# Kernel optimization log

Hardware: AMD Instinct MI355X
Metric: run time of the kernel (lower is better)

## Reference

```python
import jax, jax.numpy as jnp
import numpy as np

C, N, D, DQ, K = 8, 16384, 1024, 128, 128  # clusters, patches/cluster, feat dim, q dim, top_k per cluster


def setup_inputs() -> dict:
    key = jax.random.key(0)
    ks = jax.random.split(key, 4)
    s = 0.02
    return {
        "cluster_features": jax.random.normal(ks[0], (C, N, D), jnp.float32),
        "key_feats": jax.random.normal(ks[1], (C, 1, D), jnp.float32),
        "Wq": jax.random.normal(ks[2], (D, DQ), jnp.float32) * s,
        "bq": jnp.zeros((DQ,), jnp.float32),
        "Wv": jax.random.normal(ks[3], (D, D), jnp.float32) * s,
        "bv": jnp.zeros((D,), jnp.float32),
    }


def _ranking_topk(feats, key_feat, Wq, bq, Wv, bv):
    # feats: [n, d], key_feat: [1, d]
    Q = feats @ Wq + bq                     # [n, DQ]
    qk = key_feat @ Wq + bq                 # [1, DQ]
    A = Q @ qk.T                            # [n, 1] attention scores
    A = jax.nn.softmax(A / jnp.sqrt(jnp.float32(DQ)), axis=0)
    top_vals, top_idx = jax.lax.top_k(A[:, 0], K)   # sorted descending, like torch.topk
    top_feats = feats[top_idx]              # [K, d] gather
    V = top_feats @ Wv + bv                 # value projection on gathered subset only
    A_ = jax.nn.softmax(top_vals[:, None] / jnp.sqrt(jnp.float32(D)), axis=0)  # [K, 1]
    fusion = (A_.T @ V)[0]                  # [d] fused weighted sum
    return top_feats, fusion


def reference(cluster_features, key_feats, Wq, bq, Wv, bv):
    top_feats, fusion = jax.vmap(
        lambda f, kf: _ranking_topk(f, kf, Wq, bq, Wv, bv)
    )(cluster_features, key_feats)
    # concat per-cluster selections; C*K == num_sample_feature so no padding branch
    selected_features = top_feats.reshape(C * K, D)
    cluster_fusion_feature = fusion         # [C, D]
    return selected_features, cluster_fusion_feature
```

## Files before the change

### kernel.cpp

```cpp
#include <hip/hip_runtime.h>

#define C_CLUST 8
#define N_PAT   16384
#define D_FEAT  1024
#define DQ_DIM  128
#define K_TOP   128
#define NCHUNK  32
#define CHROWS  512

#define INV_S128 0.08838834764831844055
#define INV_S1024 0.03125

__device__ inline unsigned f2key(float f) {
    unsigned u = __float_as_uint(f);
    return (u & 0x80000000u) ? ~u : (u | 0x80000000u);
}
__device__ inline float key2f(unsigned k) {
    unsigned u = (k & 0x80000000u) ? (k ^ 0x80000000u) : ~k;
    return __uint_as_float(u);
}

__global__ __launch_bounds__(1024) void prep_kernel(
    const float* __restrict__ key_feats,
    const float* __restrict__ Wq,
    const float* __restrict__ bq,
    double* __restrict__ r,
    double* __restrict__ b0)
{
    __shared__ float keyrow[D_FEAT];
    __shared__ double part[1024];
    __shared__ double qk_lds[DQ_DIM];
    const int b = blockIdx.x;
    const int c = b >> 3, g = b & 7;
    const int tid = threadIdx.x;
    const int lane = tid & 63, wv = tid >> 6;

    keyrow[tid] = key_feats[c * D_FEAT + tid];
    __syncthreads();

    {
        const int j = tid & 127, s = tid >> 7;
        double acc = 0.0;
        for (int d = s; d < D_FEAT; d += 8)
            acc += (double)keyrow[d] * (double)Wq[d * DQ_DIM + j];
        part[s * DQ_DIM + j] = acc;
    }
    __syncthreads();
    if (tid < DQ_DIM) {
        double v = part[tid];
#pragma unroll
        for (int s2 = 1; s2 < 8; ++s2) v += part[s2 * DQ_DIM + tid];
        qk_lds[tid] = v + (double)bq[tid];
    }
    __syncthreads();

    if (g == 0 && wv == 0) {
        double p = (double)bq[lane] * qk_lds[lane] + (double)bq[64 + lane] * qk_lds[64 + lane];
#pragma unroll
        for (int o = 32; o > 0; o >>= 1) p += __shfl_xor(p, o, 64);
        if (lane == 0) b0[c] = p;
    }

    {
        const double q0 = qk_lds[lane], q1 = qk_lds[64 + lane];
        const int d0 = g * 128 + wv * 8;
#pragma unroll
        for (int i = 0; i < 8; ++i) {
            const int d = d0 + i;
            double a = (double)Wq[d * DQ_DIM + lane] * q0
                     + (double)Wq[d * DQ_DIM + 64 + lane] * q1;
#pragma unroll
            for (int o = 32; o > 0; o >>= 1) a += __shfl_xor(a, o, 64);
            if (lane == 0) r[c * D_FEAT + d] = a;
        }
    }
}

__global__ __launch_bounds__(256) void score_kernel(
    const float* __restrict__ feats,
    const double* __restrict__ r,
    const double* __restrict__ b0,
    float* __restrict__ scores)
{
    const int w    = blockIdx.x * 4 + (threadIdx.x >> 6);
    const int lane = threadIdx.x & 63;
    const int c  = w >> 10;
    const int n0 = (w & 1023) * 16;

    const double* rp = r + c * D_FEAT;
    double rr[16];
#pragma unroll
    for (int it = 0; it < 4; ++it)
#pragma unroll
        for (int j = 0; j < 4; ++j)
            rr[it * 4 + j] = rp[it * 256 + lane * 4 + j];
    const double bb = b0[c];

    const float4* fbase = (const float4*)(feats + (size_t)(c * N_PAT + n0) * D_FEAT);
    float* sout = scores + c * N_PAT + n0;

    for (int rI = 0; rI < 16; rI += 2) {
        const float4* fp0 = fbase + (size_t)(rI + 0) * 256;
        const float4* fp1 = fbase + (size_t)(rI + 1) * 256;
        double acc0 = 0.0, acc1 = 0.0;
#pragma unroll
        for (int it = 0; it < 4; ++it) {
            float4 f0 = fp0[it * 64 + lane];
            float4 f1 = fp1[it * 64 + lane];
            acc0 += (double)f0.x * rr[it * 4 + 0];
            acc0 += (double)f0.y * rr[it * 4 + 1];
            acc0 += (double)f0.z * rr[it * 4 + 2];
            acc0 += (double)f0.w * rr[it * 4 + 3];
            acc1 += (double)f1.x * rr[it * 4 + 0];
            acc1 += (double)f1.y * rr[it * 4 + 1];
            acc1 += (double)f1.z * rr[it * 4 + 2];
            acc1 += (double)f1.w * rr[it * 4 + 3];
        }
#pragma unroll
        for (int o = 32; o > 0; o >>= 1) {
            acc0 += __shfl_xor(acc0, o, 64);
            acc1 += __shfl_xor(acc1, o, 64);
        }
        if (lane == 0) {
            sout[rI + 0] = (float)(acc0 + bb);
            sout[rI + 1] = (float)(acc1 + bb);
        }
    }
}

__global__ __launch_bounds__(256) void chunksort_kernel(
    const float* __restrict__ scores,
    unsigned long long* __restrict__ cand,
    unsigned* __restrict__ mxkey,
    double* __restrict__ Ssum)
{
    const int b = blockIdx.x;
    const int c = b >> 5, chunk = b & 31;
    const int tid = threadIdx.x;
    const int lane = tid & 63, wv = tid >> 6;

    __shared__ unsigned long long su[CHROWS];
    __shared__ unsigned ured[4];
    __shared__ double dred[4];
    __shared__ unsigned bmax_s;

    const int base = c * N_PAT + chunk * CHROWS;
    const float s0 = scores[base + tid];
    const float s1 = scores[base + 256 + tid];
    const unsigned k0 = f2key(s0), k1 = f2key(s1);
    su[tid]       = ((unsigned long long)k0 << 32) | (unsigned)(~(unsigned)(chunk * CHROWS + tid));
    su[tid + 256] = ((unsigned long long)k1 << 32) | (unsigned)(~(unsigned)(chunk * CHROWS + 256 + tid));

    unsigned mk = max(k0, k1);
#pragma unroll
    for (int o = 32; o > 0; o >>= 1) mk = max(mk, __shfl_xor(mk, o, 64));
    if (lane == 0) ured[wv] = mk;
    __syncthreads();
    if (tid == 0) bmax_s = max(max(ured[0], ured[1]), max(ured[2], ured[3]));
    __syncthreads();
    const unsigned kmax = bmax_s;
    const double mx_t = (double)key2f(kmax) * INV_S128;
    double es = (double)__expf((float)((double)s0 * INV_S128 - mx_t))
              + (double)__expf((float)((double)s1 * INV_S128 - mx_t));
#pragma unroll
    for (int o = 32; o > 0; o >>= 1) es += __shfl_xor(es, o, 64);
    if (lane == 0) dred[wv] = es;
    __syncthreads();
    if (tid == 0) {
        Ssum[c * NCHUNK + chunk] = dred[0] + dred[1] + dred[2] + dred[3];
        mxkey[c * NCHUNK + chunk] = kmax;
    }

    for (int k = 2; k <= CHROWS; k <<= 1) {
        for (int j = k >> 1; j > 0; j >>= 1) {
            __syncthreads();
#pragma unroll
            for (int ii = 0; ii < 2; ++ii) {
                const int i = ii * 256 + tid, l = i ^ j;
                if (l > i) {
                    unsigned long long a = su[i], b2 = su[l];
                    const bool desc = ((i & k) == 0);
                    if (desc ? (a < b2) : (a > b2)) { su[i] = b2; su[l] = a; }
                }
            }
        }
    }
    __syncthreads();
    if (tid < K_TOP) cand[(size_t)(c * NCHUNK + chunk) * K_TOP + tid] = su[tid];
}

__global__ __launch_bounds__(256) void gather_merge_kernel(
    const float* __restrict__ feats,
    const unsigned long long* __restrict__ cand,
    const unsigned* __restrict__ mxkey,
    const double* __restrict__ Ssum,
    float* __restrict__ out,
    double* __restrict__ w_part)
{
    const int b = blockIdx.x;
    const int c = b >> 4, quarter = (b >> 2) & 3, ich = b & 3;
    const int tid = threadIdx.x;
    const int lane = tid & 63, wv = tid >> 6;

    __shared__ unsigned long long su2[4096];
    __shared__ double pd[K_TOP];
    __shared__ double sa[K_TOP];
    __shared__ int sidx[K_TOP];
    __shared__ double dred2[2];
    __shared__ double sZ;

#pragma unroll
    for (int k = 0; k < 16; ++k)
        su2[k * 256 + tid] = cand[(size_t)c * 4096 + k * 256 + tid];
    __syncthreads();

    for (int nl = 32; nl > 1; nl >>= 1) {
        const int half = nl >> 1;
        const int total = half * K_TOP;
        unsigned long long tmp[8];
        int cnt = 0;
        for (int i = tid; i < total; i += 256) {
            const int g = i >> 7, li = i & 127;
            unsigned long long a  = su2[(2 * g) * K_TOP + li];
            unsigned long long b2 = su2[(2 * g + 1) * K_TOP + (K_TOP - 1 - li)];
            tmp[cnt++] = a > b2 ? a : b2;
        }
        __syncthreads();
        cnt = 0;
        for (int i = tid; i < total; i += 256) su2[i] = tmp[cnt++];
        __syncthreads();
        for (int j = 64; j > 0; j >>= 1) {
            for (int i = tid; i < total; i += 256) {
                const int li = i & 127, l = li ^ j;
                if (l > li) {
                    const int base = i - li;
                    unsigned long long a = su2[base + li], b2 = su2[base + l];
                    if (a < b2) { su2[base + li] = b2; su2[base + l] = a; }
                }
            }
            __syncthreads();
        }
    }

    const double m_t = (double)key2f((unsigned)(su2[0] >> 32)) * INV_S128;
    if (wv == 0) {
        double z = (lane < NCHUNK)
            ? Ssum[c * NCHUNK + lane] * exp((double)key2f(mxkey[c * NCHUNK + lane]) * INV_S128 - m_t)
            : 0.0;
#pragma unroll
        for (int o = 32; o > 0; o >>= 1) z += __shfl_xor(z, o, 64);
        if (lane == 0) sZ = z;
    }
    __syncthreads();
    const double Z = sZ;
    if (tid < K_TOP) {
        unsigned long long pr = su2[tid];
        sidx[tid] = (int)(~(unsigned)(pr & 0xFFFFFFFFull));
        pd[tid] = exp((double)key2f((unsigned)(pr >> 32)) * INV_S128 - m_t) / Z;
    }
    __syncthreads();
    if (tid < K_TOP) {
        double e = exp((pd[tid] - pd[0]) * INV_S1024);
        double se = e;
#pragma unroll
        for (int o = 32; o > 0; o >>= 1) se += __shfl_xor(se, o, 64);
        if (lane == 0) dred2[wv] = se;
    }
    __syncthreads();
    if (tid < K_TOP) {
        double tot = dred2[0] + dred2[1];
        sa[tid] = exp((pd[tid] - pd[0]) * INV_S1024) / tot;
    }
    __syncthreads();

    const int d = quarter * 256 + tid;
    const float* fc = feats + (size_t)c * N_PAT * D_FEAT + d;
    float* oc = out + ((size_t)c * K_TOP + ich * 32) * D_FEAT + d;
    double a0 = 0.0, a1 = 0.0, a2 = 0.0, a3 = 0.0;
#pragma unroll 2
    for (int i = 0; i < 32; i += 4) {
        const int i0 = ich * 32 + i;
        float v0 = fc[(size_t)sidx[i0 + 0] * D_FEAT];
        float v1 = fc[(size_t)sidx[i0 + 1] * D_FEAT];
        float v2 = fc[(size_t)sidx[i0 + 2] * D_FEAT];
        float v3 = fc[(size_t)sidx[i0 + 3] * D_FEAT];
        oc[(size_t)(i + 0) * D_FEAT] = v0;
        oc[(size_t)(i + 1) * D_FEAT] = v1;
        oc[(size_t)(i + 2) * D_FEAT] = v2;
        oc[(size_t)(i + 3) * D_FEAT] = v3;
        a0 += sa[i0 + 0] * (double)v0;
        a1 += sa[i0 + 1] * (double)v1;
        a2 += sa[i0 + 2] * (double)v2;
        a3 += sa[i0 + 3] * (double)v3;
    }
    w_part[((size_t)(c * 4 + ich)) * D_FEAT + d] = (a0 + a1) + (a2 + a3);
}

__global__ __launch_bounds__(256) void fusion_kernel(
    const double* __restrict__ w_part,
    const float* __restrict__ Wv,
    const float* __restrict__ bv,
    float* __restrict__ out)
{
    __shared__ double w_lds[D_FEAT];
    __shared__ double partl[2][128];
    const int b = blockIdx.x;
    const int c = b >> 3, dpg = b & 7;
    const int tid = threadIdx.x;

    for (int d = tid; d < D_FEAT; d += 256) {
        double s = 0.0;
#pragma unroll
        for (int ich = 0; ich < 4; ++ich)
            s += w_part[((size_t)(c * 4 + ich)) * D_FEAT + d];
        w_lds[d] = s;
    }
    __syncthreads();

    const int dpl = tid & 127, half = tid >> 7;
    const int dp = dpg * 128 + dpl;
    const double* wc = w_lds + half * 512;
    const float* wvp = Wv + (size_t)(half * 512) * D_FEAT + dp;
    double a0 = 0.0, a1 = 0.0, a2 = 0.0, a3 = 0.0;
#pragma unroll 2
    for (int d = 0; d < 512; d += 4) {
        a0 += wc[d + 0] * (double)wvp[(size_t)(d + 0) * D_FEAT];
        a1 += wc[d + 1] * (double)wvp[(size_t)(d + 1) * D_FEAT];
        a2 += wc[d + 2] * (double)wvp[(size_t)(d + 2) * D_FEAT];
        a3 += wc[d + 3] * (double)wvp[(size_t)(d + 3) * D_FEAT];
    }
    partl[half][dpl] = (a0 + a1) + (a2 + a3);
    __syncthreads();
    if (half == 0) {
        double acc = (double)bv[dp] + partl[0][dpl] + partl[1][dpl];
        out[(size_t)(C_CLUST * K_TOP * D_FEAT) + c * D_FEAT + dp] = (float)acc;
    }
}

extern "C" void kernel_launch(void* const* d_in, const int* in_sizes, int n_in,
                              void* d_out, int out_size, void* d_ws, size_t ws_size,
                              hipStream_t stream) {
    const float* feats     = (const float*)d_in[0];
    const float* key_feats = (const float*)d_in[1];
    const float* Wq        = (const float*)d_in[2];
    const float* bq        = (const float*)d_in[3];
    const float* Wv        = (const float*)d_in[4];
    const float* bv        = (const float*)d_in[5];
    float* out = (float*)d_out;

    char* ws = (char*)d_ws;
    float*  scores  = (float*)(ws + 0);
    double* r       = (double*)(ws + 524288);
    double* b0      = (double*)(ws + 589824);
    unsigned long long* cand = (unsigned long long*)(ws + 589888);
    double*   Ssum  = (double*)(ws + 852032);
    unsigned* mxkey = (unsigned*)(ws + 854080);
    double*   w_part = (double*)(ws + 855104);

    hipLaunchKernelGGL(prep_kernel,         dim3(64),   dim3(1024), 0, stream,
                       key_feats, Wq, bq, r, b0);
    hipLaunchKernelGGL(score_kernel,        dim3(2048), dim3(256),  0, stream,
                       feats, r, b0, scores);
    hipLaunchKernelGGL(chunksort_kernel,    dim3(256),  dim3(256),  0, stream,
                       scores, cand, mxkey, Ssum);
    hipLaunchKernelGGL(gather_merge_kernel, dim3(128),  dim3(256),  0, stream,
                       feats, cand, mxkey, Ssum, out, w_part);
    hipLaunchKernelGGL(fusion_kernel,       dim3(64),   dim3(256),  0, stream,
                       w_part, Wv, bv, out);
}
```

Measured before the change: 230.3 us.

## Split prep kernel into parallel qk partial-sum and r projection kernels

New measurement: 193.4 us, median of 2. 16.0% less time.

```diff
diff --git a/kernel.cpp b/kernel.cpp
--- a/kernel.cpp
+++ b/kernel.cpp
@@ -20,59 +20,52 @@
     return __uint_as_float(u);
 }
 
-__global__ __launch_bounds__(1024) void prep_kernel(
+__global__ __launch_bounds__(128) void qk_kernel(
     const float* __restrict__ key_feats,
     const float* __restrict__ Wq,
+    double* __restrict__ qk_part)
+{
+    const int b = blockIdx.x;
+    const int c = b >> 4, sg = b & 15;
+    const int j = threadIdx.x;
+    const int d0 = sg * 64;
+    double acc = 0.0;
+#pragma unroll 4
+    for (int d = d0; d < d0 + 64; ++d)
+        acc += (double)key_feats[c * D_FEAT + d] * (double)Wq[d * DQ_DIM + j];
+    qk_part[(size_t)(c * 16 + sg) * DQ_DIM + j] = acc;
+}
+
+__global__ __launch_bounds__(256) void r_kernel(
+    const float* __restrict__ Wq,
     const float* __restrict__ bq,
+    const double* __restrict__ qk_part,
     double* __restrict__ r,
     double* __restrict__ b0)
 {
-    __shared__ float keyrow[D_FEAT];
-    __shared__ double part[1024];
-    __shared__ double qk_lds[DQ_DIM];
-    const int b = blockIdx.x;
-    const int c = b >> 3, g = b & 7;
-    const int tid = threadIdx.x;
-    const int lane = tid & 63, wv = tid >> 6;
-
-    keyrow[tid] = key_feats[c * D_FEAT + tid];
-    __syncthreads();
-
-    {
-        const int j = tid & 127, s = tid >> 7;
-        double acc = 0.0;
-        for (int d = s; d < D_FEAT; d += 8)
-            acc += (double)keyrow[d] * (double)Wq[d * DQ_DIM + j];
-        part[s * DQ_DIM + j] = acc;
-    }
-    __syncthreads();
-    if (tid < DQ_DIM) {
-        double v = part[tid];
-#pragma unroll
-        for (int s2 = 1; s2 < 8; ++s2) v += part[s2 * DQ_DIM + tid];
-        qk_lds[tid] = v + (double)bq[tid];
-    }
-    __syncthreads();
-
-    if (g == 0 && wv == 0) {
-        double p = (double)bq[lane] * qk_lds[lane] + (double)bq[64 + lane] * qk_lds[64 + lane];
+    const int w = blockIdx.x * 4 + (threadIdx.x >> 6);
+    const int lane = threadIdx.x & 63;
+    const int c = w >> 10, d = w & (D_FEAT - 1);
+
+    double q0 = (double)bq[lane];
+    double q1 = (double)bq[64 + lane];
+#pragma unroll
+    for (int sg = 0; sg < 16; ++sg) {
+        q0 += qk_part[(size_t)(c * 16 + sg) * DQ_DIM + lane];
+        q1 += qk_part[(size_t)(c * 16 + sg) * DQ_DIM + 64 + lane];
+    }
+
+    double a = (double)Wq[d * DQ_DIM + lane] * q0
+             + (double)Wq[d * DQ_DIM + 64 + lane] * q1;
+#pragma unroll
+    for (int o = 32; o > 0; o >>= 1) a += __shfl_xor(a, o, 64);
+    if (lane == 0) r[c * D_FEAT + d] = a;
+
+    if (d == 0) {
+        double p = (double)bq[lane] * q0 + (double)bq[64 + lane] * q1;
 #pragma unroll
         for (int o = 32; o > 0; o >>= 1) p += __shfl_xor(p, o, 64);
         if (lane == 0) b0[c] = p;
-    }
-
-    {
-        const double q0 = qk_lds[lane], q1 = qk_lds[64 + lane];
-        const int d0 = g * 128 + wv * 8;
-#pragma unroll
-        for (int i = 0; i < 8; ++i) {
-            const int d = d0 + i;
-            double a = (double)Wq[d * DQ_DIM + lane] * q0
-                     + (double)Wq[d * DQ_DIM + 64 + lane] * q1;
-#pragma unroll
-            for (int o = 32; o > 0; o >>= 1) a += __shfl_xor(a, o, 64);
-            if (lane == 0) r[c * D_FEAT + d] = a;
-        }
     }
 }
 
@@ -350,21 +343,24 @@
 
     char* ws = (char*)d_ws;
     float*  scores  = (float*)(ws + 0);
-    double* r       = (double*)(ws + 524288);
-    double* b0      = (double*)(ws + 589824);
-    unsigned long long* cand = (unsigned long long*)(ws + 589888);
-    double*   Ssum  = (double*)(ws + 852032);
-    unsigned* mxkey = (unsigned*)(ws + 854080);
-    double*   w_part = (double*)(ws + 855104);
-
-    hipLaunchKernelGGL(prep_kernel,         dim3(64),   dim3(1024), 0, stream,
-                       key_feats, Wq, bq, r, b0);
-    hipLaunchKernelGGL(score_kernel,        dim3(2048), dim3(256),  0, stream,
+    double* qk_part = (double*)(ws + 524288);
+    double* r       = (double*)(ws + 655360);
+    double* b0      = (double*)(ws + 720896);
+    unsigned long long* cand = (unsigned long long*)(ws + 720960);
+    double*   Ssum  = (double*)(ws + 983104);
+    unsigned* mxkey = (unsigned*)(ws + 985152);
+    double*   w_part = (double*)(ws + 986176);
+
+    hipLaunchKernelGGL(qk_kernel,           dim3(C_CLUST * 16), dim3(128), 0, stream,
+                       key_feats, Wq, qk_part);
+    hipLaunchKernelGGL(r_kernel,            dim3(2048), dim3(256), 0, stream,
+                       Wq, bq, qk_part, r, b0);
+    hipLaunchKernelGGL(score_kernel,        dim3(2048), dim3(256), 0, stream,
                        feats, r, b0, scores);
-    hipLaunchKernelGGL(chunksort_kernel,    dim3(256),  dim3(256),  0, stream,
+    hipLaunchKernelGGL(chunksort_kernel,    dim3(256),  dim3(256), 0, stream,
                        scores, cand, mxkey, Ssum);
-    hipLaunchKernelGGL(gather_merge_kernel, dim3(128),  dim3(256),  0, stream,
+    hipLaunchKernelGGL(gather_merge_kernel, dim3(128),  dim3(256), 0, stream,
                        feats, cand, mxkey, Ssum, out, w_part);
-    hipLaunchKernelGGL(fusion_kernel,       dim3(64),   dim3(256),  0, stream,
+    hipLaunchKernelGGL(fusion_kernel,       dim3(64),   dim3(256), 0, stream,
                        w_part, Wv, bv, out);
 }
```
